# Performance work log

Measured on AMD Instinct MI355X. Metric: run time of the kernel, lower is better.

## Reference

```python
import jax, jax.numpy as jnp
import numpy as np

B, L, D, H, DK = 2, 1024, 1024, 16, 64
LN_EPS = 1e-5


def setup_inputs() -> dict:
    key = jax.random.key(0)
    ks = jax.random.split(key, 4)
    x = jax.random.normal(ks[0], (B, L, D), dtype=jnp.float32)
    W_qkv = jax.random.normal(ks[1], (D, 3 * D), dtype=jnp.float32) * 0.02
    W_o = jax.random.normal(ks[2], (D, D), dtype=jnp.float32) * 0.02
    W_LTM = jax.random.normal(ks[3], (H, DK, DK), dtype=jnp.float32) * 0.5
    return {
        "x": x,
        "W_qkv": W_qkv,
        "W_o": W_o,
        "W_LTM": W_LTM,
        "V_gs": jnp.zeros((H,), jnp.float32),
        "V_T0": jnp.zeros((H,), jnp.float32),
        "beta_tau": jnp.ones((H,), jnp.float32),
        "beta_gm": jnp.ones((H,), jnp.float32) * 0.1,
        "C_ch": jnp.ones((H,), jnp.float32),
        "gamma": jnp.ones((H,), jnp.float32) * 0.1,
        "alpha_ppd": jnp.ones((1,), jnp.float32),
        "IC_threshold": jnp.ones((1,), jnp.float32),
        "gate": jnp.zeros((H,), jnp.float32),
    }


def _stp_physics(W_LTM, V_gs, V_T0, beta_tau, beta_gm, C_ch, alpha_ppd, IC_threshold):
    # per-head params broadcast to (H, dk, dk)
    V_eff = V_gs[:, None, None] - V_T0[:, None, None] + W_LTM  # U_T = 1.0
    sp = jax.nn.softplus(V_eff)
    g_ch = beta_tau[:, None, None] * sp
    retention = jnp.exp(-g_ch / C_ch[:, None, None])  # = 1 - Lambda
    G = beta_gm[:, None, None] * sp * jax.nn.sigmoid(V_eff)
    sign_mask = jnp.tanh(alpha_ppd * (g_ch - IC_threshold))
    return retention, G, sign_mask


def reference(x, W_qkv, W_o, W_LTM, V_gs, V_T0, beta_tau, beta_gm, C_ch,
              gamma, alpha_ppd, IC_threshold, gate):
    Bb, Ll, Dd = x.shape
    qkv = (x @ W_qkv).reshape(Bb, Ll, 3, H, DK)
    q, k, v = qkv[:, :, 0], qkv[:, :, 1], qkv[:, :, 2]  # (B,L,H,dk)

    # LayerNorm over dk, no affine
    mu = jnp.mean(k, axis=-1, keepdims=True)
    var = jnp.var(k, axis=-1, keepdims=True)
    k_normed = (k - mu) * jax.lax.rsqrt(var + LN_EPS)

    # ---- causal softmax attention ----
    scale = 1.0 / np.sqrt(DK)
    attn = jnp.einsum('bihd,bjhd->bhij', q, k) * scale
    causal = jnp.tril(jnp.ones((Ll, Ll), dtype=bool))
    attn = jnp.where(causal[None, None], attn, -jnp.inf)
    attn = jax.nn.softmax(attn, axis=-1)
    softmax_out = jnp.einsum('bhij,bjhd->bihd', attn, v)  # (B,L,H,dk)

    # ---- STP fast-weight recurrence ----
    retention, G, sign_mask = _stp_physics(W_LTM, V_gs, V_T0, beta_tau,
                                           beta_gm, C_ch, alpha_ppd, IC_threshold)
    coeff = gamma[:, None, None] * sign_mask * G  # (H,dk,dk)

    def step(F_state, qkv_t):
        q_t, k_t, v_t = qkv_t  # (B,H,dk) each; k_t is normed
        hebbian = jnp.einsum('bhd,bhe->bhde', v_t, k_t)
        F_new = retention[None] * F_state + coeff[None] * hebbian
        y_t = jnp.einsum('bhde,bhe->bhd', W_LTM[None] + F_new, q_t)
        return F_new, y_t

    xs = (jnp.moveaxis(q, 1, 0), jnp.moveaxis(k_normed, 1, 0), jnp.moveaxis(v, 1, 0))
    F0 = jnp.zeros((Bb, H, DK, DK), dtype=x.dtype)
    _, ys = jax.lax.scan(step, F0, xs)
    stp_out = jnp.moveaxis(ys, 0, 1)  # (B,L,H,dk)

    g = jax.nn.sigmoid(gate)[None, None, :, None]
    y = g * softmax_out + (1.0 - g) * stp_out
    y = y.reshape(Bb, Ll, Dd)
    return y @ W_o
```

## Files before the change

kernel.cpp:

```cpp
#include <hip/hip_runtime.h>
#include <hip/hip_bf16.h>
#include <math.h>

#define LQ 1024
#define DH 1024
#define NH 16
#define DKH 64

typedef __bf16 bf16x8 __attribute__((ext_vector_type(8)));
typedef float f32x4 __attribute__((ext_vector_type(4)));
typedef const unsigned int __attribute__((address_space(1)))* gas1_t;
typedef unsigned int __attribute__((address_space(3)))* las3_t;

__device__ __forceinline__ unsigned pack2bf(float a, float b) {
  union { __hip_bfloat16 h[2]; unsigned u; } t;
  t.h[0] = __float2bfloat16(a);
  t.h[1] = __float2bfloat16(b);
  return t.u;
}
__device__ __forceinline__ unsigned short bfbits(float x) {
  __hip_bfloat16 h = __float2bfloat16(x);
  return *(unsigned short*)&h;
}
__device__ __forceinline__ void bf4w(float* dst, uint2 r) {
  dst[0] = __uint_as_float(r.x << 16);
  dst[1] = __uint_as_float(r.x & 0xffff0000u);
  dst[2] = __uint_as_float(r.y << 16);
  dst[3] = __uint_as_float(r.y & 0xffff0000u);
}

__global__ __launch_bounds__(256) void prep_kernel(
    const float* __restrict__ x, const float* __restrict__ W_qkv, const float* __restrict__ W_o,
    const float* __restrict__ W_LTM, const float* __restrict__ V_gs, const float* __restrict__ V_T0,
    const float* __restrict__ beta_tau, const float* __restrict__ beta_gm, const float* __restrict__ C_ch,
    const float* __restrict__ gamma_, const float* __restrict__ alpha_ppd, const float* __restrict__ IC_thr,
    const float* __restrict__ gate,
    __hip_bfloat16* __restrict__ xb, __hip_bfloat16* __restrict__ wqt, __hip_bfloat16* __restrict__ wot,
    float* __restrict__ ret, float* __restrict__ ret64, float* __restrict__ co, float* __restrict__ g_out) {
  __shared__ float ts[32][33];
  const int bx = blockIdx.x, tid = threadIdx.x;
  if (bx < 256) {
    int idx = bx * 256 + tid;
    int h = idx >> 12;
    float w = W_LTM[idx];
    float veff = V_gs[h] - V_T0[h] + w;
    float sp = fmaxf(veff, 0.f) + log1pf(expf(-fabsf(veff)));
    float gch = beta_tau[h] * sp;
    float e1 = gch / C_ch[h];
    float sig = 1.f / (1.f + expf(-veff));
    float G = beta_gm[h] * sp * sig;
    float sm = tanhf(alpha_ppd[0] * (gch - IC_thr[0]));
    ret[idx] = expf(-e1);
    ret64[idx] = expf(-64.f * e1);
    co[idx] = gamma_[h] * sm * G;
    if (idx < NH) g_out[idx] = 1.f / (1.f + expf(-gate[idx]));
  } else if (bx < 2304) {
    size_t i = (size_t)((bx - 256) * 256 + tid) * 4;
    float4 v = *(const float4*)(x + i);
    __hip_bfloat16 t[4] = {__float2bfloat16(v.x), __float2bfloat16(v.y),
                           __float2bfloat16(v.z), __float2bfloat16(v.w)};
    *(uint2*)(xb + i) = *(uint2*)t;
  } else {
    const float* W;
    __hip_bfloat16* Wt;
    int n0, k0, N;
    if (bx < 5376) {
      int idx = bx - 2304;
      W = W_qkv; Wt = wqt; N = 3072;
      n0 = (idx % 96) * 32; k0 = (idx / 96) * 32;
    } else {
      int idx = bx - 5376;
      W = W_o; Wt = wot; N = 1024;
      n0 = (idx & 31) * 32; k0 = (idx >> 5) * 32;
    }
    int r = tid >> 5, c = tid & 31;
#pragma unroll
    for (int i = 0; i < 4; i++) ts[r + 8 * i][c] = W[(size_t)(k0 + r + 8 * i) * N + n0 + c];
    __syncthreads();
#pragma unroll
    for (int i = 0; i < 4; i++)
      Wt[(size_t)(n0 + r + 8 * i) * 1024 + k0 + c] = __float2bfloat16(ts[c][r + 8 * i]);
  }
}

__global__ __launch_bounds__(256) void gemm_qkv_kernel(
    const __hip_bfloat16* __restrict__ A, const __hip_bfloat16* __restrict__ Bt,
    __hip_bfloat16* __restrict__ C, __hip_bfloat16* __restrict__ knb,
    __hip_bfloat16* __restrict__ vt, int M, int N, int K) {
  __shared__ union {
    struct { unsigned short As[64 * 32]; unsigned short Bs[128 * 32]; } ab;
    unsigned short Vt[4][64][36];
  } sm;
  const int tid = threadIdx.x;
  const int w = tid >> 6, lane = tid & 63;
  const int quad = lane >> 4, l16 = lane & 15;
  const int wm = w & 1, wn = w >> 1;
  const int row0 = blockIdx.y * 64, col0 = blockIdx.x * 128;
  const int sr = lane >> 2;
  const int sk = (lane & 3) * 8;
  f32x4 acc[2][4];
#pragma unroll
  for (int i = 0; i < 2; i++)
#pragma unroll
    for (int j = 0; j < 4; j++) acc[i][j] = (f32x4){0.f, 0.f, 0.f, 0.f};

  for (int k0 = 0; k0 < K; k0 += 32) {
    __syncthreads();
    {
      const __hip_bfloat16* gA = A + (size_t)(row0 + w * 16 + sr) * K + k0 + sk;
      __builtin_amdgcn_global_load_lds((gas1_t)gA, (las3_t)((char*)sm.ab.As + w * 1024), 16, 0, 0);
#pragma unroll
      for (int c = 0; c < 2; c++) {
        int s = c * 4 + w;
        const __hip_bfloat16* gB = Bt + (size_t)(col0 + s * 16 + sr) * K + k0 + sk;
        __builtin_amdgcn_global_load_lds((gas1_t)gB, (las3_t)((char*)sm.ab.Bs + s * 1024), 16, 0, 0);
      }
    }
    __syncthreads();
    bf16x8 af[2], bfr[4];
#pragma unroll
    for (int i = 0; i < 2; i++)
      af[i] = *(const bf16x8*)((const char*)sm.ab.As + (((wm * 32 + i * 16 + l16) * 32 + quad * 8) << 1));
#pragma unroll
    for (int j = 0; j < 4; j++)
      bfr[j] = *(const bf16x8*)((const char*)sm.ab.Bs + (((wn * 64 + j * 16 + l16) * 32 + quad * 8) << 1));
#pragma unroll
    for (int i = 0; i < 2; i++)
#pragma unroll
      for (int j = 0; j < 4; j++)
        acc[i][j] = __builtin_amdgcn_mfma_f32_16x16x32_bf16(af[i], bfr[j], acc[i][j], 0, 0, 0);
  }
#pragma unroll
  for (int i = 0; i < 2; i++) {
    int rowb = row0 + wm * 32 + i * 16 + quad * 4;
#pragma unroll
    for (int j = 0; j < 4; j++) {
      int col = col0 + wn * 64 + j * 16 + l16;
#pragma unroll
      for (int r = 0; r < 4; r++)
        C[(size_t)(rowb + r) * N + col] = __float2bfloat16(acc[i][j][r]);
    }
  }
  const int sec = col0 >> 10;
  const int hh = ((col0 & 1023) >> 6) + wn;
  if (sec == 1) {
#pragma unroll
    for (int i = 0; i < 2; i++) {
      f32x4 s1 = {0.f, 0.f, 0.f, 0.f}, s2 = {0.f, 0.f, 0.f, 0.f};
#pragma unroll
      for (int j = 0; j < 4; j++)
#pragma unroll
        for (int r = 0; r < 4; r++) {
          s1[r] += acc[i][j][r];
          s2[r] += acc[i][j][r] * acc[i][j][r];
        }
#pragma unroll
      for (int m = 1; m <= 8; m <<= 1)
#pragma unroll
        for (int r = 0; r < 4; r++) {
          s1[r] += __shfl_xor(s1[r], m);
          s2[r] += __shfl_xor(s2[r], m);
        }
#pragma unroll
      for (int r = 0; r < 4; r++) {
        float mu = s1[r] * (1.f / 64.f);
        float var = s2[r] * (1.f / 64.f) - mu * mu;
        float inv = rsqrtf(var + 1e-5f);
        int row = row0 + wm * 32 + i * 16 + quad * 4 + r;
#pragma unroll
        for (int j = 0; j < 4; j++)
          knb[((size_t)row * NH + hh) * DKH + j * 16 + l16] = __float2bfloat16((acc[i][j][r] - mu) * inv);
      }
    }
  } else if (sec == 2) {
    __syncthreads();
#pragma unroll
    for (int i = 0; i < 2; i++)
#pragma unroll
      for (int j = 0; j < 4; j++)
#pragma unroll
        for (int r = 0; r < 4; r++)
          sm.Vt[w][j * 16 + l16][i * 16 + quad * 4 + r] = bfbits(acc[i][j][r]);
    const int b = row0 >> 10;
    const int t0 = (row0 & 1023) + wm * 32;
    const int bh = b * NH + hh;
    const int cc = lane & 3, ddl = lane >> 2;
#pragma unroll
    for (int pass = 0; pass < 4; pass++) {
      int d = pass * 16 + ddl;
      uint2 a0 = *(const uint2*)&sm.Vt[w][d][cc * 8];
      uint2 a1 = *(const uint2*)&sm.Vt[w][d][cc * 8 + 4];
      uint4 val = {a0.x, a0.y, a1.x, a1.y};
      *(uint4*)(vt + ((size_t)bh * DKH + d) * LQ + t0 + cc * 8) = val;
    }
  }
}

__global__ __launch_bounds__(256) void gemm_out_kernel(
    const __hip_bfloat16* __restrict__ A, const __hip_bfloat16* __restrict__ Bt,
    float* __restrict__ C, int M, int N, int K) {
  __shared__ unsigned short As[8 * 512];
  __shared__ unsigned short Bs[8 * 512];
  const int tid = threadIdx.x;
  const int w = tid >> 6, lane = tid & 63;
  const int quad = lane >> 4, l16 = lane & 15;
  const int wm = w & 1, wn = w >> 1;
  const int row0 = blockIdx.y * 64, col0 = blockIdx.x * 64;
  const int fr = lane & 15;
  const int fk = (lane >> 4) * 8;
  f32x4 acc[2][2];
#pragma unroll
  for (int i = 0; i < 2; i++)
#pragma unroll
    for (int j = 0; j < 2; j++) acc[i][j] = (f32x4){0.f, 0.f, 0.f, 0.f};

  for (int k0 = 0; k0 < K; k0 += 64) {
    __syncthreads();
#pragma unroll
    for (int kk = 0; kk < 2; kk++) {
      const int f = kk * 4 + w;
      const __hip_bfloat16* gA = A + (size_t)(row0 + w * 16 + fr) * K + k0 + kk * 32 + fk;
      __builtin_amdgcn_global_load_lds((gas1_t)gA, (las3_t)((char*)As + f * 1024), 16, 0, 0);
      const __hip_bfloat16* gB = Bt + (size_t)(col0 + w * 16 + fr) * K + k0 + kk * 32 + fk;
      __builtin_amdgcn_global_load_lds((gas1_t)gB, (las3_t)((char*)Bs + f * 1024), 16, 0, 0);
    }
    __syncthreads();
#pragma unroll
    for (int kk = 0; kk < 2; kk++) {
      bf16x8 af[2], bfr[2];
#pragma unroll
      for (int i = 0; i < 2; i++)
        af[i] = *(const bf16x8*)((const char*)As + (((kk * 4 + wm * 2 + i) * 64 + lane) << 4));
#pragma unroll
      for (int j = 0; j < 2; j++)
        bfr[j] = *(const bf16x8*)((const char*)Bs + (((kk * 4 + wn * 2 + j) * 64 + lane) << 4));
#pragma unroll
      for (int i = 0; i < 2; i++)
#pragma unroll
        for (int j = 0; j < 2; j++)
          acc[i][j] = __builtin_amdgcn_mfma_f32_16x16x32_bf16(af[i], bfr[j], acc[i][j], 0, 0, 0);
    }
  }
#pragma unroll
  for (int i = 0; i < 2; i++) {
    int rowb = row0 + wm * 32 + i * 16 + quad * 4;
#pragma unroll
    for (int j = 0; j < 2; j++) {
      int col = col0 + wn * 32 + j * 16 + l16;
#pragma unroll
      for (int r = 0; r < 4; r++)
        C[(size_t)(rowb + r) * N + col] = acc[i][j][r];
    }
  }
}

__global__ __launch_bounds__(256) void attn_state_kernel(
    const __hip_bfloat16* __restrict__ qkvb, const __hip_bfloat16* __restrict__ vt,
    __hip_bfloat16* __restrict__ sob, const __hip_bfloat16* __restrict__ knb,
    const float* __restrict__ ret_g, const float* __restrict__ co_g, float* __restrict__ S) {
  __shared__ __attribute__((aligned(16))) union {
    struct { __hip_bfloat16 Ks[8 * 64 * 8]; __hip_bfloat16 Vs[8 * 64 * 8]; } at;
    struct { float kb[2][8][64]; float vb[2][8][64]; } st;
  } sm;
  const int bx = blockIdx.x;
  const int tid = threadIdx.x;
  if (bx < 512) {
    const int it = 15 - (bx & 15);
    const int h = (bx >> 4) & 15, b = bx >> 8;
    const int bh = b * NH + h;
    const int w = tid >> 6, lane = tid & 63;
    const int l16 = lane & 15, quad = lane >> 4;
    const int i0 = it * 64;
    const int q_abs = i0 + w * 16 + l16;
    bf16x8 aq[2];
    aq[0] = *(const bf16x8*)(qkvb + (size_t)(b * LQ + q_abs) * 3 * DH + h * DKH + quad * 8);
    aq[1] = *(const bf16x8*)(qkvb + (size_t)(b * LQ + q_abs) * 3 * DH + h * DKH + 32 + quad * 8);
    f32x4 o[4];
#pragma unroll
    for (int dt = 0; dt < 4; dt++) o[dt] = (f32x4){0.f, 0.f, 0.f, 0.f};
    float mrun = -3e38f, lrun = 0.f;

    for (int jt = 0; jt <= it; jt++) {
      const int j0 = jt * 64;
      __syncthreads();
#pragma unroll
      for (int ff = 0; ff < 2; ff++) {
        const int f = w * 2 + ff;
        const int nt = f >> 1, kk = f & 1;
        const __hip_bfloat16* gk = qkvb + (size_t)(b * LQ + j0 + nt * 16 + l16) * 3 * DH + DH +
                                   h * DKH + kk * 32 + quad * 8;
        __builtin_amdgcn_global_load_lds((gas1_t)gk, (las3_t)(sm.at.Ks + f * 512), 16, 0, 0);
        const __hip_bfloat16* gv = vt + ((size_t)bh * DKH + nt * 16 + l16) * LQ + j0 + kk * 32 + quad * 8;
        __builtin_amdgcn_global_load_lds((gas1_t)gv, (las3_t)(sm.at.Vs + f * 512), 16, 0, 0);
      }
      __syncthreads();
      f32x4 s[4];
#pragma unroll
      for (int nt = 0; nt < 4; nt++) s[nt] = (f32x4){0.f, 0.f, 0.f, 0.f};
#pragma unroll
      for (int kk = 0; kk < 2; kk++)
#pragma unroll
        for (int nt = 0; nt < 4; nt++) {
          bf16x8 bk = *(const bf16x8*)(sm.at.Ks + ((nt * 2 + kk) * 64 + lane) * 8);
          s[nt] = __builtin_amdgcn_mfma_f32_16x16x32_bf16(bk, aq[kk], s[nt], 0, 0, 0);
        }
#pragma unroll
      for (int nt = 0; nt < 4; nt++)
#pragma unroll
        for (int r = 0; r < 4; r++) {
          float sv = s[nt][r] * 0.125f;
          if (jt == it && (j0 + nt * 16 + quad * 4 + r > q_abs)) sv = -1e30f;
          s[nt][r] = sv;
        }
      float mx = -3e38f;
#pragma unroll
      for (int nt = 0; nt < 4; nt++)
#pragma unroll
        for (int r = 0; r < 4; r++) mx = fmaxf(mx, s[nt][r]);
      mx = fmaxf(mx, __shfl_xor(mx, 16));
      mx = fmaxf(mx, __shfl_xor(mx, 32));
      float mn = fmaxf(mrun, mx);
      float al = __expf(mrun - mn);
      mrun = mn;
      float p[4][4];
      float rs = 0.f;
#pragma unroll
      for (int nt = 0; nt < 4; nt++)
#pragma unroll
        for (int r = 0; r < 4; r++) {
          float pv = __expf(s[nt][r] - mn);
          p[nt][r] = pv;
          rs += pv;
        }
      rs += __shfl_xor(rs, 16);
      rs += __shfl_xor(rs, 32);
      lrun = lrun * al + rs;
      unsigned pk[4][2];
#pragma unroll
      for (int nt = 0; nt < 4; nt++) {
        pk[nt][0] = pack2bf(p[nt][0], p[nt][1]);
        pk[nt][1] = pack2bf(p[nt][2], p[nt][3]);
      }
      const int srcA = l16 | ((quad & 1) << 5);
      const bool hi_sel = (quad >> 1) != 0;
      bf16x8 ap[2];
#pragma unroll
      for (int kk = 0; kk < 2; kk++) {
        union { unsigned u[4]; bf16x8 v; } cv;
#pragma unroll
        for (int gi = 0; gi < 2; gi++) {
          int src = srcA + (gi << 4);
          unsigned lo0 = (unsigned)__shfl((int)pk[kk * 2][0], src);
          unsigned lo1 = (unsigned)__shfl((int)pk[kk * 2][1], src);
          unsigned hi0 = (unsigned)__shfl((int)pk[kk * 2 + 1][0], src);
          unsigned hi1 = (unsigned)__shfl((int)pk[kk * 2 + 1][1], src);
          cv.u[gi * 2] = hi_sel ? hi0 : lo0;
          cv.u[gi * 2 + 1] = hi_sel ? hi1 : lo1;
        }
        ap[kk] = cv.v;
      }
#pragma unroll
      for (int dt = 0; dt < 4; dt++)
#pragma unroll
        for (int r = 0; r < 4; r++) o[dt][r] *= al;
#pragma unroll
      for (int kk = 0; kk < 2; kk++)
#pragma unroll
        for (int dt = 0; dt < 4; dt++) {
          bf16x8 bv = *(const bf16x8*)(sm.at.Vs + ((dt * 2 + kk) * 64 + lane) * 8);
          o[dt] = __builtin_amdgcn_mfma_f32_16x16x32_bf16(bv, ap[kk], o[dt], 0, 0, 0);
        }
    }
    float inv = 1.f / lrun;
    __hip_bfloat16* ob = sob + ((size_t)(b * LQ + q_abs) * NH + h) * DKH + quad * 4;
#pragma unroll
    for (int dt = 0; dt < 4; dt++) {
      uint2 val = {pack2bf(o[dt][0] * inv, o[dt][1] * inv),
                   pack2bf(o[dt][2] * inv, o[dt][3] * inv)};
      *(uint2*)(ob + dt * 16) = val;
    }
  } else {
    const int sx = bx - 512;
    const int c = sx >> 6;
    const int xr = sx & 63;
    const int bh = xr >> 1;
    const int half = xr & 1;
    const int bb = bh >> 4, h = bh & 15;
    const int dl = tid >> 3, j = tid & 7;
    const int d = half * 32 + dl;
    float F[8], R[8], Cc[8];
    const int base = h * 4096 + d * 64 + j * 8;
#pragma unroll
    for (int i = 0; i < 8; i++) {
      F[i] = 0.f;
      R[i] = ret_g[base + i];
      Cc[i] = co_g[base + i];
    }
    const int t00 = c * 64;
    const int sten = tid >> 7;
    const int sli = tid & 127;
    const int ss = sli >> 4;
    const int se = (sli & 15) * 4;
    {
      int t = t00 + ss;
      uint2 raw = (sten == 0)
          ? *(const uint2*)(knb + ((size_t)(bb * LQ + t) * NH + h) * DKH + se)
          : *(const uint2*)(qkvb + ((size_t)(bb * LQ + t) * 3 + 2) * DH + h * DKH + se);
      bf4w(sten == 0 ? &sm.st.kb[0][ss][se] : &sm.st.vb[0][ss][se], raw);
    }
    __syncthreads();
    for (int sc = 0; sc < 8; sc++) {
      const int p = sc & 1;
      uint2 raw;
      if (sc < 7) {
        int t = t00 + (sc + 1) * 8 + ss;
        raw = (sten == 0)
            ? *(const uint2*)(knb + ((size_t)(bb * LQ + t) * NH + h) * DKH + se)
            : *(const uint2*)(qkvb + ((size_t)(bb * LQ + t) * 3 + 2) * DH + h * DKH + se);
      }
#pragma unroll
      for (int s = 0; s < 8; s++) {
        float vd = sm.st.vb[p][s][d];
        float4 k0 = *(const float4*)&sm.st.kb[p][s][j * 8];
        float4 k1 = *(const float4*)&sm.st.kb[p][s][j * 8 + 4];
        float ke[8] = {k0.x, k0.y, k0.z, k0.w, k1.x, k1.y, k1.z, k1.w};
#pragma unroll
        for (int i = 0; i < 8; i++) F[i] = fmaf(Cc[i] * vd, ke[i], R[i] * F[i]);
      }
      if (sc < 7) bf4w(sten == 0 ? &sm.st.kb[p ^ 1][ss][se] : &sm.st.vb[p ^ 1][ss][se], raw);
      __syncthreads();
    }
    const size_t sb = ((size_t)c * 2048 + ((size_t)bb * 16 + h) * 64 + d) * 64 + j * 8;
#pragma unroll
    for (int i = 0; i < 8; i++) S[sb + i] = F[i];
  }
}

__global__ __launch_bounds__(256) void scan_out_kernel(
    const __hip_bfloat16* __restrict__ qkvb, const __hip_bfloat16* __restrict__ knb,
    const float* __restrict__ W_LTM, const float* __restrict__ ret_g, const float* __restrict__ co_g,
    const float* __restrict__ S, const float* __restrict__ ret64,
    const __hip_bfloat16* __restrict__ sob, const float* __restrict__ g,
    __hip_bfloat16* __restrict__ mixb) {
  const int bh = blockIdx.x >> 1;
  const int half = blockIdx.x & 1;
  const int c = 15 - blockIdx.y;
  const int bb = bh >> 4, h = bh & 15;
  const int tid = threadIdx.x;
  const int dl = tid >> 3, j = tid & 7;
  const int d = half * 32 + dl;
  const float gh = g[h];
  float F[8], R[8], Cc[8], W[8];
  const int base = h * 4096 + d * 64 + j * 8;
#pragma unroll
  for (int i = 0; i < 8; i++) {
    F[i] = 0.f;
    R[i] = ret_g[base + i];
    Cc[i] = co_g[base + i];
    W[i] = W_LTM[base + i];
  }
  if (c > 0) {
    float r64v[8];
#pragma unroll
    for (int i = 0; i < 8; i++) r64v[i] = ret64[base + i];
    const size_t srow = (((size_t)bb * 16 + h) * 64 + d) * 64 + j * 8;
    for (int cb = 0; cb < c; cb += 8) {
      float4 b0[8], b1[8];
#pragma unroll
      for (int t = 0; t < 8; t++) {
        if (cb + t < c) {
          const float* sp = S + (size_t)(cb + t) * 131072 + srow;
          b0[t] = *(const float4*)sp;
          b1[t] = *(const float4*)(sp + 4);
        }
      }
#pragma unroll
      for (int t = 0; t < 8; t++) {
        if (cb + t < c) {
          float sv[8] = {b0[t].x, b0[t].y, b0[t].z, b0[t].w, b1[t].x, b1[t].y, b1[t].z, b1[t].w};
#pragma unroll
          for (int i = 0; i < 8; i++) F[i] = fmaf(r64v[i], F[i], sv[i]);
        }
      }
    }
  }
  __shared__ float qb[2][8][64], kb[2][8][64], vb[2][8][64];
  const int t00 = c * 64;
  const int sten = tid >> 7;
  const int sli = tid & 127;
  const int ss = sli >> 4;
  const int se = (sli & 15) * 4;
  const int vs = tid >> 5;
  const int ve = (tid & 31) * 2;
  {
    int t = t00 + ss, tv = t00 + vs;
    uint2 rqk = (sten == 0)
        ? *(const uint2*)(qkvb + (size_t)(bb * LQ + t) * 3 * DH + h * DKH + se)
        : *(const uint2*)(knb + ((size_t)(bb * LQ + t) * NH + h) * DKH + se);
    unsigned rv = *(const unsigned*)(qkvb + ((size_t)(bb * LQ + tv) * 3 + 2) * DH + h * DKH + ve);
    bf4w(sten == 0 ? &qb[0][ss][se] : &kb[0][ss][se], rqk);
    vb[0][vs][ve] = __uint_as_float(rv << 16);
    vb[0][vs][ve + 1] = __uint_as_float(rv & 0xffff0000u);
  }
  __syncthreads();
  for (int sc = 0; sc < 8; sc++) {
    const int p = sc & 1;
    uint2 rqk;
    unsigned rv;
    if (sc < 7) {
      int t = t00 + (sc + 1) * 8 + ss, tv = t00 + (sc + 1) * 8 + vs;
      rqk = (sten == 0)
          ? *(const uint2*)(qkvb + (size_t)(bb * LQ + t) * 3 * DH + h * DKH + se)
          : *(const uint2*)(knb + ((size_t)(bb * LQ + t) * NH + h) * DKH + se);
      rv = *(const unsigned*)(qkvb + ((size_t)(bb * LQ + tv) * 3 + 2) * DH + h * DKH + ve);
    }
    float ykeep = 0.f;
#pragma unroll
    for (int s = 0; s < 8; s++) {
      float vd = vb[p][s][d];
      float4 k0 = *(const float4*)&kb[p][s][j * 8];
      float4 k1 = *(const float4*)&kb[p][s][j * 8 + 4];
      float4 q0 = *(const float4*)&qb[p][s][j * 8];
      float4 q1 = *(const float4*)&qb[p][s][j * 8 + 4];
      float ke[8] = {k0.x, k0.y, k0.z, k0.w, k1.x, k1.y, k1.z, k1.w};
      float qe[8] = {q0.x, q0.y, q0.z, q0.w, q1.x, q1.y, q1.z, q1.w};
      float yp = 0.f;
#pragma unroll
      for (int i = 0; i < 8; i++) {
        F[i] = fmaf(Cc[i] * vd, ke[i], R[i] * F[i]);
        yp = fmaf(W[i] + F[i], qe[i], yp);
      }
      yp += __shfl_xor(yp, 1);
      yp += __shfl_xor(yp, 2);
      yp += __shfl_xor(yp, 4);
      if (j == s) ykeep = yp;
    }
    {
      const size_t oi = ((size_t)(bb * LQ + t00 + sc * 8 + j) * NH + h) * DKH + d;
      float sv = __bfloat162float(sob[oi]);
      mixb[oi] = __float2bfloat16(gh * sv + (1.f - gh) * ykeep);
    }
    if (sc < 7) {
      bf4w(sten == 0 ? &qb[p ^ 1][ss][se] : &kb[p ^ 1][ss][se], rqk);
      vb[p ^ 1][vs][ve] = __uint_as_float(rv << 16);
      vb[p ^ 1][vs][ve + 1] = __uint_as_float(rv & 0xffff0000u);
    }
    __syncthreads();
  }
}

extern "C" void kernel_launch(void* const* d_in, const int* in_sizes, int n_in,
                              void* d_out, int out_size, void* d_ws, size_t ws_size,
                              hipStream_t stream) {
  (void)in_sizes; (void)n_in; (void)out_size; (void)ws_size;
  const float* x        = (const float*)d_in[0];
  const float* W_qkv    = (const float*)d_in[1];
  const float* W_o      = (const float*)d_in[2];
  const float* W_LTM    = (const float*)d_in[3];
  const float* V_gs     = (const float*)d_in[4];
  const float* V_T0     = (const float*)d_in[5];
  const float* beta_tau = (const float*)d_in[6];
  const float* beta_gm  = (const float*)d_in[7];
  const float* C_ch     = (const float*)d_in[8];
  const float* gamma_   = (const float*)d_in[9];
  const float* alpha_p  = (const float*)d_in[10];
  const float* IC_thr   = (const float*)d_in[11];
  const float* gate     = (const float*)d_in[12];

  float* ws  = (float*)d_ws;
  __hip_bfloat16* qkvb = (__hip_bfloat16*)ws;
  __hip_bfloat16* knb  = (__hip_bfloat16*)(ws + 3145728);
  __hip_bfloat16* sob  = (__hip_bfloat16*)(ws + 4194304);
  __hip_bfloat16* mixb = (__hip_bfloat16*)(ws + 5242880);
  __hip_bfloat16* vtb  = (__hip_bfloat16*)(ws + 6291456);
  __hip_bfloat16* xb   = (__hip_bfloat16*)(ws + 7340032);
  __hip_bfloat16* wqt  = (__hip_bfloat16*)(ws + 8388608);
  __hip_bfloat16* wot  = (__hip_bfloat16*)(ws + 9961472);
  float* ret   = ws + 10485760;
  float* ret64 = ret + 65536;
  float* co    = ret64 + 65536;
  float* g     = co + 65536;
  float* Sbuf  = g + 64;
  float* out = (float*)d_out;

  prep_kernel<<<6400, 256, 0, stream>>>(x, W_qkv, W_o, W_LTM, V_gs, V_T0, beta_tau, beta_gm,
                                        C_ch, gamma_, alpha_p, IC_thr, gate,
                                        xb, wqt, wot, ret, ret64, co, g);
  gemm_qkv_kernel<<<dim3(24, 32), 256, 0, stream>>>(xb, wqt, qkvb, knb, vtb, 2048, 3072, 1024);
  attn_state_kernel<<<1472, 256, 0, stream>>>(qkvb, vtb, sob, knb, ret, co, Sbuf);
  scan_out_kernel<<<dim3(64, 16), 256, 0, stream>>>(qkvb, knb, W_LTM, ret, co, Sbuf, ret64, sob, g, mixb);
  gemm_out_kernel<<<dim3(16, 32), 256, 0, stream>>>(mixb, wot, out, 2048, 1024, 1024);
}
```

Measured before the change: 194.9 us.

## Stage whole 64-step chunk in LDS once instead of double-buffered 8-step slices

Both the chunk-state kernel and the scan-output kernel now load all 64 timesteps of k, v (and q) into shared memory in a single batch, then run the recurrence with no per-8-step syncs or prefetch. V is kept as raw bf16 in LDS to save space. In the scan kernel the chunk load is issued before the inter-chunk state prefix over S, so it overlaps that global traffic. This removes eight barriers and the interleaved prefetch logic per block. The cost is more LDS per block (about 40KB in the scan kernel), which may lower occupancy.

```diff
diff --git a/kernel.cpp b/kernel.cpp
--- a/kernel.cpp
+++ b/kernel.cpp
@@ -260,7 +260,7 @@
     const float* __restrict__ ret_g, const float* __restrict__ co_g, float* __restrict__ S) {
   __shared__ __attribute__((aligned(16))) union {
     struct { __hip_bfloat16 Ks[8 * 64 * 8]; __hip_bfloat16 Vs[8 * 64 * 8]; } at;
-    struct { float kb[2][8][64]; float vb[2][8][64]; } st;
+    struct { float kb[64][64]; unsigned short vb[64][64]; } st;
   } sm;
   const int bx = blockIdx.x;
   const int tid = threadIdx.x;
@@ -397,38 +397,29 @@
       Cc[i] = co_g[base + i];
     }
     const int t00 = c * 64;
-    const int sten = tid >> 7;
-    const int sli = tid & 127;
-    const int ss = sli >> 4;
-    const int se = (sli & 15) * 4;
-    {
-      int t = t00 + ss;
-      uint2 raw = (sten == 0)
-          ? *(const uint2*)(knb + ((size_t)(bb * LQ + t) * NH + h) * DKH + se)
-          : *(const uint2*)(qkvb + ((size_t)(bb * LQ + t) * 3 + 2) * DH + h * DKH + se);
-      bf4w(sten == 0 ? &sm.st.kb[0][ss][se] : &sm.st.vb[0][ss][se], raw);
-    }
-    __syncthreads();
-    for (int sc = 0; sc < 8; sc++) {
-      const int p = sc & 1;
-      uint2 raw;
-      if (sc < 7) {
-        int t = t00 + (sc + 1) * 8 + ss;
-        raw = (sten == 0)
-            ? *(const uint2*)(knb + ((size_t)(bb * LQ + t) * NH + h) * DKH + se)
-            : *(const uint2*)(qkvb + ((size_t)(bb * LQ + t) * 3 + 2) * DH + h * DKH + se);
-      }
-#pragma unroll
-      for (int s = 0; s < 8; s++) {
-        float vd = sm.st.vb[p][s][d];
-        float4 k0 = *(const float4*)&sm.st.kb[p][s][j * 8];
-        float4 k1 = *(const float4*)&sm.st.kb[p][s][j * 8 + 4];
-        float ke[8] = {k0.x, k0.y, k0.z, k0.w, k1.x, k1.y, k1.z, k1.w};
-#pragma unroll
-        for (int i = 0; i < 8; i++) F[i] = fmaf(Cc[i] * vd, ke[i], R[i] * F[i]);
-      }
-      if (sc < 7) bf4w(sten == 0 ? &sm.st.kb[p ^ 1][ss][se] : &sm.st.vb[p ^ 1][ss][se], raw);
-      __syncthreads();
+    uint2 kr[4], vr[4];
+#pragma unroll
+    for (int i = 0; i < 4; i++) {
+      int idx = (tid + 256 * i) * 4;
+      int s = idx >> 6, e = idx & 63;
+      kr[i] = *(const uint2*)(knb + ((size_t)(bb * LQ + t00 + s) * NH + h) * DKH + e);
+      vr[i] = *(const uint2*)(qkvb + ((size_t)(bb * LQ + t00 + s) * 3 + 2) * DH + h * DKH + e);
+    }
+#pragma unroll
+    for (int i = 0; i < 4; i++) {
+      int idx = (tid + 256 * i) * 4;
+      int s = idx >> 6, e = idx & 63;
+      bf4w(&sm.st.kb[s][e], kr[i]);
+      *(uint2*)&sm.st.vb[s][e] = vr[i];
+    }
+    __syncthreads();
+    for (int t = 0; t < 64; t++) {
+      float vd = __uint_as_float((unsigned)sm.st.vb[t][d] << 16);
+      float4 k0 = *(const float4*)&sm.st.kb[t][j * 8];
+      float4 k1 = *(const float4*)&sm.st.kb[t][j * 8 + 4];
+      float ke[8] = {k0.x, k0.y, k0.z, k0.w, k1.x, k1.y, k1.z, k1.w};
+#pragma unroll
+      for (int i = 0; i < 8; i++) F[i] = fmaf(Cc[i] * vd, ke[i], R[i] * F[i]);
     }
     const size_t sb = ((size_t)c * 2048 + ((size_t)bb * 16 + h) * 64 + d) * 64 + j * 8;
 #pragma unroll
@@ -442,6 +433,11 @@
     const float* __restrict__ S, const float* __restrict__ ret64,
     const __hip_bfloat16* __restrict__ sob, const float* __restrict__ g,
     __hip_bfloat16* __restrict__ mixb) {
+  __shared__ __attribute__((aligned(16))) struct {
+    float qb[64][64];
+    float kb[64][64];
+    unsigned short vb[64][64];
+  } sm;
   const int bh = blockIdx.x >> 1;
   const int half = blockIdx.x & 1;
   const int c = 15 - blockIdx.y;
@@ -459,6 +455,26 @@
     Cc[i] = co_g[base + i];
     W[i] = W_LTM[base + i];
   }
+  const int t00 = c * 64;
+  {
+    uint2 qr[4], kr[4], vr[4];
+#pragma unroll
+    for (int i = 0; i < 4; i++) {
+      int idx = (tid + 256 * i) * 4;
+      int s = idx >> 6, e = idx & 63;
+      qr[i] = *(const uint2*)(qkvb + (size_t)(bb * LQ + t00 + s) * 3 * DH + h * DKH + e);
+      kr[i] = *(const uint2*)(knb + ((size_t)(bb * LQ + t00 + s) * NH + h) * DKH + e);
+      vr[i] = *(const uint2*)(qkvb + ((size_t)(bb * LQ + t00 + s) * 3 + 2) * DH + h * DKH + e);
+    }
+#pragma unroll
+    for (int i = 0; i < 4; i++) {
+      int idx = (tid + 256 * i) * 4;
+      int s = idx >> 6, e = idx & 63;
+      bf4w(&sm.qb[s][e], qr[i]);
+      bf4w(&sm.kb[s][e], kr[i]);
+      *(uint2*)&sm.vb[s][e] = vr[i];
+    }
+  }
   if (c > 0) {
     float r64v[8];
 #pragma unroll
@@ -484,44 +500,17 @@
       }
     }
   }
-  __shared__ float qb[2][8][64], kb[2][8][64], vb[2][8][64];
-  const int t00 = c * 64;
-  const int sten = tid >> 7;
-  const int sli = tid & 127;
-  const int ss = sli >> 4;
-  const int se = (sli & 15) * 4;
-  const int vs = tid >> 5;
-  const int ve = (tid & 31) * 2;
-  {
-    int t = t00 + ss, tv = t00 + vs;
-    uint2 rqk = (sten == 0)
-        ? *(const uint2*)(qkvb + (size_t)(bb * LQ + t) * 3 * DH + h * DKH + se)
-        : *(const uint2*)(knb + ((size_t)(bb * LQ + t) * NH + h) * DKH + se);
-    unsigned rv = *(const unsigned*)(qkvb + ((size_t)(bb * LQ + tv) * 3 + 2) * DH + h * DKH + ve);
-    bf4w(sten == 0 ? &qb[0][ss][se] : &kb[0][ss][se], rqk);
-    vb[0][vs][ve] = __uint_as_float(rv << 16);
-    vb[0][vs][ve + 1] = __uint_as_float(rv & 0xffff0000u);
-  }
   __syncthreads();
   for (int sc = 0; sc < 8; sc++) {
-    const int p = sc & 1;
-    uint2 rqk;
-    unsigned rv;
-    if (sc < 7) {
-      int t = t00 + (sc + 1) * 8 + ss, tv = t00 + (sc + 1) * 8 + vs;
-      rqk = (sten == 0)
-          ? *(const uint2*)(qkvb + (size_t)(bb * LQ + t) * 3 * DH + h * DKH + se)
-          : *(const uint2*)(knb + ((size_t)(bb * LQ + t) * NH + h) * DKH + se);
-      rv = *(const unsigned*)(qkvb + ((size_t)(bb * LQ + tv) * 3 + 2) * DH + h * DKH + ve);
-    }
     float ykeep = 0.f;
 #pragma unroll
     for (int s = 0; s < 8; s++) {
-      float vd = vb[p][s][d];
-      float4 k0 = *(const float4*)&kb[p][s][j * 8];
-      float4 k1 = *(const float4*)&kb[p][s][j * 8 + 4];
-      float4 q0 = *(const float4*)&qb[p][s][j * 8];
-      float4 q1 = *(const float4*)&qb[p][s][j * 8 + 4];
+      const int t = sc * 8 + s;
+      float vd = __uint_as_float((unsigned)sm.vb[t][d] << 16);
+      float4 k0 = *(const float4*)&sm.kb[t][j * 8];
+      float4 k1 = *(const float4*)&sm.kb[t][j * 8 + 4];
+      float4 q0 = *(const float4*)&sm.qb[t][j * 8];
+      float4 q1 = *(const float4*)&sm.qb[t][j * 8 + 4];
       float ke[8] = {k0.x, k0.y, k0.z, k0.w, k1.x, k1.y, k1.z, k1.w};
       float qe[8] = {q0.x, q0.y, q0.z, q0.w, q1.x, q1.y, q1.z, q1.w};
       float yp = 0.f;
@@ -540,12 +529,6 @@
       float sv = __bfloat162float(sob[oi]);
       mixb[oi] = __float2bfloat16(gh * sv + (1.f - gh) * ykeep);
     }
-    if (sc < 7) {
-      bf4w(sten == 0 ? &qb[p ^ 1][ss][se] : &kb[p ^ 1][ss][se], rqk);
-      vb[p ^ 1][vs][ve] = __uint_as_float(rv << 16);
-      vb[p ^ 1][vs][ve + 1] = __uint_as_float(rv & 0xffff0000u);
-    }
-    __syncthreads();
   }
 }
 
```

Result: no change. 198.5 us (+1.8%).
